# Optimization experiments

Measured on AMD Instinct MI355X. Metric: run time of the kernel, lower is better.

## Reference

```python
import jax, jax.numpy as jnp
import numpy as np

NUM_CLASSES = 21
TOP_K = 200
VAR0, VAR1 = 0.1, 0.2
CONF_THRESH = 0.01
NMS_THRESH = 0.45
NUM_PRIORS = 3000
BATCH = 256


def _decode(loc, priors):
    # loc, priors: [P, 4] (cx, cy, w, h) -> corner boxes [P, 4]
    cxcy = priors[:, :2] + loc[:, :2] * VAR0 * priors[:, 2:]
    wh = priors[:, 2:] * jnp.exp(loc[:, 2:] * VAR1)
    return jnp.concatenate([cxcy - wh * 0.5, cxcy + wh * 0.5], axis=1)


def _iou_one_vs_all(box, boxes):
    # box [4], boxes [P,4] corner form
    lt = jnp.maximum(box[:2], boxes[:, :2])
    rb = jnp.minimum(box[2:], boxes[:, 2:])
    wh = jnp.clip(rb - lt, 0.0)
    inter = wh[:, 0] * wh[:, 1]
    area1 = (box[2] - box[0]) * (box[3] - box[1])
    area2 = (boxes[:, 2] - boxes[:, 0]) * (boxes[:, 3] - boxes[:, 1])
    return inter / (area1 + area2 - inter)


def _nms_one_class(boxes, scores):
    # boxes [P,4], scores [P] -> [TOP_K, 5] rows of (score, x1, y1, x2, y2)
    neg_inf = jnp.array(-jnp.inf, boxes.dtype)
    sc0 = jnp.where(scores > CONF_THRESH, scores, neg_inf)

    def step(sc, _):
        i = jnp.argmax(sc)
        s = sc[i]
        b = boxes[i]
        valid = s > CONF_THRESH
        iou = _iou_one_vs_all(b, boxes)
        sc = jnp.where(iou > NMS_THRESH, neg_inf, sc).at[i].set(neg_inf)
        row = jnp.where(valid, jnp.concatenate([s[None], b]), jnp.zeros(5, boxes.dtype))
        return sc, row

    _, rows = jax.lax.scan(step, sc0, None, length=TOP_K)
    return rows


def setup_inputs() -> dict:
    key = jax.random.key(0)
    k1, k2, k3 = jax.random.split(key, 3)
    loc_data = jax.random.normal(k1, (BATCH, NUM_PRIORS, 4), dtype=jnp.float32)
    conf_data = jax.random.uniform(k2, (BATCH, NUM_PRIORS, NUM_CLASSES), dtype=jnp.float32)
    pr = jax.random.uniform(k3, (NUM_PRIORS, 4), dtype=jnp.float32)
    # centers in [0,1], widths/heights in [0.05, 0.5]
    priors = jnp.concatenate([pr[:, :2], 0.05 + 0.45 * pr[:, 2:]], axis=1)
    return {"loc_data": loc_data, "conf_data": conf_data, "priors": priors}


def reference(loc_data, conf_data, priors):
    # decode per image: [B, P, 4]
    decoded = jax.vmap(lambda l: _decode(l, priors))(loc_data)
    # class-major scores, skipping background class 0: [B, C-1, P]
    cls_scores = jnp.transpose(conf_data, (0, 2, 1))[:, 1:, :]
    per_bc = jax.vmap(jax.vmap(_nms_one_class, in_axes=(None, 0)),
                      in_axes=(0, 0))(decoded, cls_scores)  # [B, C-1, TOP_K, 5]
    bg = jnp.zeros((loc_data.shape[0], 1, TOP_K, 5), loc_data.dtype)
    return jnp.concatenate([bg, per_bc], axis=1)  # [B, C, TOP_K, 5]
```

## Files before the change

kernel.cpp:

```cpp
#include <hip/hip_runtime.h>
#include <math.h>


#define NCLS 21
#define TOPK 200
#define NPRI 3000
#define ELTS 47
#define CONF_T 0.01f
#define MHI 0.45f
#define MLO 1.490116119384765625e-08f
#define CAP 256
#define NBUCK 256
#define NUSED 224
#define BITS_BASE 0x3C000000u
#define BSHIFT 18

__device__ __forceinline__ float rdlf(float v, int l) {
  return __int_as_float(__builtin_amdgcn_readlane(__float_as_int(v), l));
}

__device__ __forceinline__ float iou_val(const float4 k, const float a,
                                         const float4 b, const float carea) {
  float ltx = fmaxf(k.x, b.x), lty = fmaxf(k.y, b.y);
  float rbx = fminf(k.z, b.z), rby = fminf(k.w, b.w);
  float iw = fmaxf(rbx - ltx, 0.0f), ih = fmaxf(rby - lty, 0.0f);
  float inter = iw * ih;
  float uni = (a + carea) - inter;
  return fmaf(-MLO, uni, fmaf(-MHI, uni, inter));
}

__device__ __forceinline__ bool iou_sup(const float4 k, const float a,
                                        const float4 b, const float carea) {
  return iou_val(k, a, b, carea) > 0.0f;
}

__device__ __forceinline__ int resolve_tile(
    unsigned long long smask, const float4 bx, const float carea,
    const unsigned int bits, const int lane, int nk,
    float4* kbox, float* karr, float* kscore) {
  unsigned long long M = ~smask;
  while (M && nk < TOPK) {
    const int ls = (int)__builtin_ctzll(M);
    const float sx1 = rdlf(bx.x, ls), sy1 = rdlf(bx.y, ls);
    const float sx2 = rdlf(bx.z, ls), sy2 = rdlf(bx.w, ls);
    const float sar = rdlf(carea, ls);
    const unsigned int sbits =
        (unsigned int)__builtin_amdgcn_readlane((int)bits, ls);
    const float4 nb = make_float4(sx1, sy1, sx2, sy2);
    if (lane == 0) {
      kbox[nk]   = nb;
      karr[nk]   = sar;
      kscore[nk] = __uint_as_float(sbits);
    }
    ++nk;
    M &= ~__ballot(iou_val(nb, sar, bx, carea) > 0.0f);
    M &= ~(1ull << ls);
  }
  return nk;
}

__global__ __launch_bounds__(128, 8) void ssd_nms_kernel(
    const float* __restrict__ loc, const float* __restrict__ conf,
    const float* __restrict__ priors, float* __restrict__ out, int nbatch) {
  const int blk = blockIdx.x;
  int b, c1;
  if ((nbatch & 7) == 0) {
    const int xcd  = blk & 7;
    const int rest = blk >> 3;
    b  = (rest / 20) * 8 + xcd;
    c1 = rest % 20;
  } else {
    b  = blk / 20;
    c1 = blk % 20;
  }
  const int c    = 1 + c1;
  const int tid  = threadIdx.x;
  const int lane = tid & 63;
  const int w    = tid >> 6;

  __shared__ unsigned long long skey[CAP];
  __shared__ unsigned int hist[NBUCK / 2];
  __shared__ float4 kbox[TOPK];
  __shared__ alignas(16) float karr[TOPK];
  __shared__ float  kscore[TOPK];
  __shared__ int sh_nk;
  __shared__ int sh_ctr;

  if (c1 == 0) {
    float* o0 = out + (size_t)b * NCLS * TOPK * 5;
    for (int i = tid; i < TOPK * 5; i += 128) o0[i] = 0.0f;
  }

  for (int i = tid; i < NBUCK / 2; i += 128) hist[i] = 0u;
  if (tid == 0) sh_nk = 0;
  __syncthreads();

  const float* myF = conf + (size_t)b * NPRI * NCLS + c;
  const float4* myL = (const float4*)loc + (size_t)b * NPRI;
  const float4* pri4 = (const float4*)priors;

  for (int k = w; k < ELTS; k += 2) {
    const int j = k * 64 + lane;
    unsigned int bits = 0u;
    if (j < NPRI) {
      float s = myF[(size_t)j * NCLS];
      bits = (s > CONF_T) ? __float_as_uint(s) : 0u;
    }
    if (bits) {
      unsigned int bu = (bits - BITS_BASE) >> BSHIFT;
      atomicAdd(&hist[bu >> 1], 1u << ((bu & 1) * 16));
    }
  }
  __syncthreads();

  float* obase = out + ((size_t)b * NCLS + c) * (TOPK * 5);
  int cutHiB = NUSED;

  for (;;) {
    if (sh_nk >= TOPK || cutHiB <= 0) break;

    int sl = 0;
#pragma unroll
    for (int t = 0; t < 4; ++t) {
      int bu = lane * 4 + t;
      if (bu < cutHiB) sl += (int)((hist[bu >> 1] >> ((bu & 1) * 16)) & 0xFFFFu);
    }
    int suf = sl;
#pragma unroll
    for (int d = 1; d < 64; d <<= 1) {
      int v = __shfl_down(suf, d, 64);
      if (lane + d < 64) suf += v;
    }
    unsigned long long m = __ballot(suf <= CAP);
    int Ls = (m != 0ull) ? __builtin_ctzll(m) : 63;
    int cutLoB = Ls * 4;
    if (cutLoB >= cutHiB) cutLoB = (cutHiB - 1) & ~3;
    const unsigned int loBits = BITS_BASE + ((unsigned)cutLoB << BSHIFT);
    const unsigned int hiBits = BITS_BASE + ((unsigned)cutHiB << BSHIFT);

    if (tid == 0) sh_ctr = 0;
    for (int t = tid; t < CAP; t += 128) skey[t] = 0ull;
    __syncthreads();

    for (int k = w; k < ELTS; k += 2) {
      const int j = k * 64 + lane;
      unsigned int bits = 0u;
      if (j < NPRI) {
        float s = myF[(size_t)j * NCLS];
        bits = (s > CONF_T) ? __float_as_uint(s) : 0u;
      }
      bool sel = (bits >= loBits) && (bits < hiBits);
      unsigned long long bm = __ballot(sel);
      int cnt = (int)__popcll(bm);
      int wb = 0;
      if (lane == 0 && cnt) wb = atomicAdd(&sh_ctr, cnt);
      wb = __builtin_amdgcn_readfirstlane(wb);
      if (sel) {
        int pos = wb + (int)__popcll(bm & ((1ull << lane) - 1ull));
        if (pos < CAP)
          skey[pos] = ((unsigned long long)bits << 12) | (unsigned)(4095 - j);
      }
    }
    __syncthreads();
    int Nc = sh_ctr;
    if (Nc > CAP) Nc = CAP;

    if (Nc > 0) {
      for (int kk = 2; kk <= CAP; kk <<= 1) {
        for (int jj = kk >> 1; jj > 0; jj >>= 1) {
          if (jj == 128) __syncthreads();
          int i = ((tid & ~(jj - 1)) << 1) | (tid & (jj - 1));
          int ixj = i | jj;
          unsigned long long a = skey[i], d = skey[ixj];
          bool up = (i & kk) == 0;
          if (up ? (a < d) : (a > d)) { skey[i] = d; skey[ixj] = a; }
          if (jj == 128) __syncthreads();
          else __threadfence_block();
        }
      }
      __syncthreads();

      for (int p0 = 0;; p0 += 128) {
        if (p0 >= Nc) break;
        const int nk0 = sh_nk;
        if (nk0 >= TOPK) break;

        const int p = p0 + w * 64 + lane;
        const bool valid = p < Nc;
        unsigned long long key = valid ? skey[p] : 0ull;
        unsigned int bits = (unsigned int)(key >> 12);
        int j = 4095 - (int)(key & 4095ull);

        const int jg = valid ? j : 0;
        const float4 l4 = myL[jg];
        const float4 pp = pri4[jg];
        float cx = pp.x + (l4.x * 0.1f) * pp.z;
        float cy = pp.y + (l4.y * 0.1f) * pp.w;
        float bw = pp.z * expf(l4.z * 0.2f);
        float bh = pp.w * expf(l4.w * 0.2f);
        float4 bx = make_float4(cx - bw * 0.5f, cy - bh * 0.5f,
                                cx + bw * 0.5f, cy + bh * 0.5f);
        float carea = (bx.z - bx.x) * (bx.w - bx.y);

        float fm = valid ? -1.0f : 1.0f;
        int s = 0;
        for (; s + 3 < nk0; s += 4) {
          float4 k0 = kbox[s];     float4 k1 = kbox[s + 1];
          float4 k2 = kbox[s + 2]; float4 k3 = kbox[s + 3];
          float4 ar = *(const float4*)&karr[s];
          float v01 = fmaxf(iou_val(k0, ar.x, bx, carea),
                            iou_val(k1, ar.y, bx, carea));
          float v23 = fmaxf(iou_val(k2, ar.z, bx, carea),
                            iou_val(k3, ar.w, bx, carea));
          fm = fmaxf(fm, fmaxf(v01, v23));
          if (__ballot(fm > 0.0f) == ~0ull) { s = nk0; break; }
        }
        for (; s < nk0; ++s)
          fm = fmaxf(fm, iou_val(kbox[s], karr[s], bx, carea));
        unsigned long long smask = __ballot(fm > 0.0f);

        if (w == 0) {
          int nk = resolve_tile(smask, bx, carea, bits, lane, nk0,
                                kbox, karr, kscore);
          if (lane == 0) sh_nk = nk;
        }
        __syncthreads();
        if (w == 1) {
          const int nk1 = sh_nk;
          for (int s2 = nk0; s2 < nk1; ++s2) {
            smask |= __ballot(iou_sup(kbox[s2], karr[s2], bx, carea));
            if (smask == ~0ull) break;
          }
          int nk = resolve_tile(smask, bx, carea, bits, lane, nk1,
                                kbox, karr, kscore);
          if (lane == 0) sh_nk = nk;
        }
        __syncthreads();
      }
    }
    cutHiB = cutLoB;
  }

  __syncthreads();
  const int nkf = sh_nk;
  const float* kbf = (const float*)&kbox[0];
  for (int i = tid; i < TOPK * 5; i += 128) {
    int r = i / 5;
    int col = i - r * 5;
    float v = 0.0f;
    if (r < nkf) v = (col == 0) ? kscore[r] : kbf[r * 4 + (col - 1)];
    obase[i] = v;
  }
}

extern "C" void kernel_launch(void* const* d_in, const int* in_sizes, int n_in,
                              void* d_out, int out_size, void* d_ws, size_t ws_size,
                              hipStream_t stream) {
  const float* loc    = (const float*)d_in[0];
  const float* conf   = (const float*)d_in[1];
  const float* priors = (const float*)d_in[2];
  float* out = (float*)d_out;
  (void)d_ws; (void)ws_size;

  const int batch = in_sizes[0] / (NPRI * 4);
  hipLaunchKernelGGL(ssd_nms_kernel, dim3(batch * 20), dim3(128), 0, stream,
                     loc, conf, priors, out, batch);
}
```

Measured before the change: 421.2 us.

## Bucket-sort candidate indices into workspace list to avoid rescanning scores per pass

After building the score histogram, the kernel computes per-bucket prefix offsets and scatters each above-threshold prior index into a per-(batch,class) global workspace list ordered by bucket. Each refill pass then gathers only the candidates for the selected bucket range from that list, instead of rescanning all 3000 strided conf scores with ballots and atomics. This adds one extra full scan plus global scatter writes and gathers, and falls back to the old path when the workspace is too small.

Result: no change. 418.0 us (-0.8%).

```diff
diff --git a/kernel.cpp b/kernel.cpp
--- a/kernel.cpp
+++ b/kernel.cpp
@@ -61,7 +61,8 @@
 
 __global__ __launch_bounds__(128, 8) void ssd_nms_kernel(
     const float* __restrict__ loc, const float* __restrict__ conf,
-    const float* __restrict__ priors, float* __restrict__ out, int nbatch) {
+    const float* __restrict__ priors, float* __restrict__ out,
+    unsigned short* __restrict__ jlist, int nbatch, int useL) {
   const int blk = blockIdx.x;
   int b, c1;
   if ((nbatch & 7) == 0) {
@@ -80,6 +81,8 @@
 
   __shared__ unsigned long long skey[CAP];
   __shared__ unsigned int hist[NBUCK / 2];
+  __shared__ unsigned short pfx[NUSED + 2];
+  __shared__ unsigned int ctr[NUSED];
   __shared__ float4 kbox[TOPK];
   __shared__ alignas(16) float karr[TOPK];
   __shared__ float  kscore[TOPK];
@@ -98,6 +101,7 @@
   const float* myF = conf + (size_t)b * NPRI * NCLS + c;
   const float4* myL = (const float4*)loc + (size_t)b * NPRI;
   const float4* pri4 = (const float4*)priors;
+  unsigned short* jl = jlist + ((size_t)b * 20 + c1) * NPRI;
 
   for (int k = w; k < ELTS; k += 2) {
     const int j = k * 64 + lane;
@@ -113,57 +117,129 @@
   }
   __syncthreads();
 
+  if (useL) {
+    if (w == 0) {
+      const int bu0 = lane * 4;
+      int c0 = 0, c1x = 0, c2 = 0, c3 = 0;
+      if (bu0 < NUSED) {
+        unsigned int h0 = hist[lane * 2];
+        unsigned int h1 = hist[lane * 2 + 1];
+        c0 = (int)(h0 & 0xFFFFu); c1x = (int)(h0 >> 16);
+        c2 = (int)(h1 & 0xFFFFu); c3 = (int)(h1 >> 16);
+      }
+      const int sl = c0 + c1x + c2 + c3;
+      int incl = sl;
+#pragma unroll
+      for (int d = 1; d < 64; d <<= 1) {
+        int v = __shfl_up(incl, d, 64);
+        if (lane >= d) incl += v;
+      }
+      const int excl = incl - sl;
+      if (bu0 < NUSED) {
+        pfx[bu0]     = (unsigned short)excl;
+        pfx[bu0 + 1] = (unsigned short)(excl + c0);
+        pfx[bu0 + 2] = (unsigned short)(excl + c0 + c1x);
+        pfx[bu0 + 3] = (unsigned short)(excl + c0 + c1x + c2);
+      }
+      if (lane == 56) pfx[NUSED] = (unsigned short)excl;
+    }
+    __syncthreads();
+    for (int i = tid; i < NUSED; i += 128) ctr[i] = pfx[i];
+    __syncthreads();
+
+    for (int k = w; k < ELTS; k += 2) {
+      const int j = k * 64 + lane;
+      if (j < NPRI) {
+        float s = myF[(size_t)j * NCLS];
+        if (s > CONF_T) {
+          unsigned int bits = __float_as_uint(s);
+          unsigned int bu = (bits - BITS_BASE) >> BSHIFT;
+          unsigned int pos = atomicAdd(&ctr[bu], 1u);
+          jl[pos] = (unsigned short)j;
+        }
+      }
+    }
+    __syncthreads();
+  }
+
   float* obase = out + ((size_t)b * NCLS + c) * (TOPK * 5);
   int cutHiB = NUSED;
 
   for (;;) {
     if (sh_nk >= TOPK || cutHiB <= 0) break;
 
-    int sl = 0;
+    int Nc, lo = 0;
+    int cutLoB;
+    if (useL) {
+      const int bu = lane * 4;
+      int suf = 0;
+      if (bu < cutHiB) suf = (int)pfx[cutHiB] - (int)pfx[bu];
+      unsigned long long m = __ballot(suf <= CAP);
+      int Ls = (m != 0ull) ? __builtin_ctzll(m) : 63;
+      cutLoB = Ls * 4;
+      if (cutLoB >= cutHiB) cutLoB = (cutHiB - 1) & ~3;
+      lo = (int)pfx[cutLoB];
+      Nc = (int)pfx[cutHiB] - lo;
+      if (Nc > CAP) Nc = CAP;
+
+      if (Nc > 0) {
+        for (int t = tid; t < CAP; t += 128) {
+          unsigned long long key = 0ull;
+          if (t < Nc) {
+            const int j = (int)jl[lo + t];
+            const unsigned int bits = __float_as_uint(myF[(size_t)j * NCLS]);
+            key = ((unsigned long long)bits << 12) | (unsigned)(4095 - j);
+          }
+          skey[t] = key;
+        }
+        __syncthreads();
+      }
+    } else {
+      int sl = 0;
 #pragma unroll
-    for (int t = 0; t < 4; ++t) {
-      int bu = lane * 4 + t;
-      if (bu < cutHiB) sl += (int)((hist[bu >> 1] >> ((bu & 1) * 16)) & 0xFFFFu);
-    }
-    int suf = sl;
+      for (int t = 0; t < 4; ++t) {
+        int bu = lane * 4 + t;
+        if (bu < cutHiB) sl += (int)((hist[bu >> 1] >> ((bu & 1) * 16)) & 0xFFFFu);
+      }
+      int suf = sl;
 #pragma unroll
-    for (int d = 1; d < 64; d <<= 1) {
-      int v = __shfl_down(suf, d, 64);
-      if (lane + d < 64) suf += v;
-    }
-    unsigned long long m = __ballot(suf <= CAP);
-    int Ls = (m != 0ull) ? __builtin_ctzll(m) : 63;
-    int cutLoB = Ls * 4;
-    if (cutLoB >= cutHiB) cutLoB = (cutHiB - 1) & ~3;
-    const unsigned int loBits = BITS_BASE + ((unsigned)cutLoB << BSHIFT);
-    const unsigned int hiBits = BITS_BASE + ((unsigned)cutHiB << BSHIFT);
-
-    if (tid == 0) sh_ctr = 0;
-    for (int t = tid; t < CAP; t += 128) skey[t] = 0ull;
-    __syncthreads();
-
-    for (int k = w; k < ELTS; k += 2) {
-      const int j = k * 64 + lane;
-      unsigned int bits = 0u;
-      if (j < NPRI) {
-        float s = myF[(size_t)j * NCLS];
-        bits = (s > CONF_T) ? __float_as_uint(s) : 0u;
-      }
-      bool sel = (bits >= loBits) && (bits < hiBits);
-      unsigned long long bm = __ballot(sel);
-      int cnt = (int)__popcll(bm);
-      int wb = 0;
-      if (lane == 0 && cnt) wb = atomicAdd(&sh_ctr, cnt);
-      wb = __builtin_amdgcn_readfirstlane(wb);
-      if (sel) {
-        int pos = wb + (int)__popcll(bm & ((1ull << lane) - 1ull));
-        if (pos < CAP)
-          skey[pos] = ((unsigned long long)bits << 12) | (unsigned)(4095 - j);
-      }
-    }
-    __syncthreads();
-    int Nc = sh_ctr;
-    if (Nc > CAP) Nc = CAP;
+      for (int d = 1; d < 64; d <<= 1) {
+        int v = __shfl_down(suf, d, 64);
+        if (lane + d < 64) suf += v;
+      }
+      unsigned long long m = __ballot(suf <= CAP);
+      int Ls = (m != 0ull) ? __builtin_ctzll(m) : 63;
+      cutLoB = Ls * 4;
+      if (cutLoB >= cutHiB) cutLoB = (cutHiB - 1) & ~3;
+      const unsigned int loBits = BITS_BASE + ((unsigned)cutLoB << BSHIFT);
+      const unsigned int hiBits = BITS_BASE + ((unsigned)cutHiB << BSHIFT);
+
+      if (tid == 0) sh_ctr = 0;
+      for (int t = tid; t < CAP; t += 128) skey[t] = 0ull;
+      __syncthreads();
+      for (int k = w; k < ELTS; k += 2) {
+        const int j = k * 64 + lane;
+        unsigned int bits = 0u;
+        if (j < NPRI) {
+          float s = myF[(size_t)j * NCLS];
+          bits = (s > CONF_T) ? __float_as_uint(s) : 0u;
+        }
+        bool sel = (bits >= loBits) && (bits < hiBits);
+        unsigned long long bm = __ballot(sel);
+        int cnt = (int)__popcll(bm);
+        int wb = 0;
+        if (lane == 0 && cnt) wb = atomicAdd(&sh_ctr, cnt);
+        wb = __builtin_amdgcn_readfirstlane(wb);
+        if (sel) {
+          int pos = wb + (int)__popcll(bm & ((1ull << lane) - 1ull));
+          if (pos < CAP)
+            skey[pos] = ((unsigned long long)bits << 12) | (unsigned)(4095 - j);
+        }
+      }
+      __syncthreads();
+      Nc = sh_ctr;
+      if (Nc > CAP) Nc = CAP;
+    }
 
     if (Nc > 0) {
       for (int kk = 2; kk <= CAP; kk <<= 1) {
@@ -260,9 +336,12 @@
   const float* conf   = (const float*)d_in[1];
   const float* priors = (const float*)d_in[2];
   float* out = (float*)d_out;
-  (void)d_ws; (void)ws_size;
 
   const int batch = in_sizes[0] / (NPRI * 4);
+  unsigned short* jlist = (unsigned short*)d_ws;
+  const size_t need = (size_t)batch * 20 * NPRI * sizeof(unsigned short);
+  const int useL = (d_ws != nullptr && ws_size >= need) ? 1 : 0;
+
   hipLaunchKernelGGL(ssd_nms_kernel, dim3(batch * 20), dim3(128), 0, stream,
-                     loc, conf, priors, out, batch);
-}
+                     loc, conf, priors, out, jlist, batch, useL);
+}
```
